# Kernel optimization log

Measured on AMD Instinct MI355X. Metric: run time of the kernel, lower is better.

## Reference

```python
import jax, jax.numpy as jnp
import numpy as np
from jax import lax

PART = 224   # PART_IMAGE_SIZE
PAD = 224    # PAD_SIZE
TOPN = 4
IOU_THRESH = 0.25
N_ANCHORS = 1614


def _conv(x, w, b, stride, pad):
    y = lax.conv_general_dilated(x, w, (stride, stride), [(pad, pad), (pad, pad)],
                                 dimension_numbers=('NCHW', 'OIHW', 'NCHW'))
    return y + b[None, :, None, None]


def _iou(box, boxes):
    # box [4], boxes [N,4] as (y0,x0,y1,x1)
    yy0 = jnp.maximum(box[0], boxes[:, 0]); xx0 = jnp.maximum(box[1], boxes[:, 1])
    yy1 = jnp.minimum(box[2], boxes[:, 2]); xx1 = jnp.minimum(box[3], boxes[:, 3])
    inter = jnp.clip(yy1 - yy0, 0.0) * jnp.clip(xx1 - xx0, 0.0)
    a = (box[2] - box[0]) * (box[3] - box[1])
    areas = (boxes[:, 2] - boxes[:, 0]) * (boxes[:, 3] - boxes[:, 1])
    return inter / (a + areas - inter)


def _nms(scores, boxes):
    # hard NMS keeping TOPN boxes; returns indices [TOPN]
    valid = jnp.ones(scores.shape, dtype=bool)
    idxs = []
    for _ in range(TOPN):
        i = jnp.argmax(jnp.where(valid, scores, -jnp.inf))
        idxs.append(i)
        valid = valid & (_iou(boxes[i], boxes) <= IOU_THRESH)
    return jnp.stack(idxs)


def _crop_resize(img, box):
    # img [3,Hp,Wp] padded image, box [4] float; bilinear, align_corners=True,
    # matching F.interpolate(x_pad[:, :, y0:y1, x0:x1], (PART, PART))
    Hp, Wp = img.shape[1], img.shape[2]
    def coords(c0, c1, L):
        t = jnp.arange(PART, dtype=img.dtype) / (PART - 1)
        c = c0 + (c1 - 1.0 - c0) * t          # absolute source coordinate
        cf = jnp.floor(c)
        lo = jnp.clip(cf.astype(jnp.int32), 0, L - 1)
        hi = jnp.clip(lo + 1, 0, L - 1)
        return lo, hi, c - cf
    yl, yh, wy = coords(box[0], box[2], Hp)
    xl, xh, wx = coords(box[1], box[3], Wp)
    g = lambda yi, xi: img[:, yi[:, None], xi[None, :]]   # [3,PART,PART]
    return ((1 - wy)[:, None] * ((1 - wx) * g(yl, xl) + wx * g(yl, xh))
            + wy[:, None] * ((1 - wx) * g(yh, xl) + wx * g(yh, xh)))


def setup_inputs() -> dict:
    key = jax.random.key(0)
    ks = jax.random.split(key, 20)
    x = jax.random.uniform(ks[0], (16, 3, 448, 448), dtype=jnp.float32)
    rpn_feature = jax.random.normal(ks[1], (16, 2048, 14, 14), dtype=jnp.float32)
    # valid boxes inside the padded 896x896 image
    y0 = jax.random.randint(ks[2], (N_ANCHORS,), 0, 560)
    x0 = jax.random.randint(ks[3], (N_ANCHORS,), 0, 560)
    h = jax.random.randint(ks[4], (N_ANCHORS,), 32, 336)
    w = jax.random.randint(ks[5], (N_ANCHORS,), 32, 336)
    anchors = jnp.stack([y0, x0, jnp.minimum(y0 + h, 896), jnp.minimum(x0 + w, 896)], axis=1).astype(jnp.int32)
    s = 0.02
    inp = {
        'x': x, 'rpn_feature': rpn_feature, 'anchors': anchors,
        'w_down1': jax.random.normal(ks[6], (128, 2048, 3, 3), jnp.float32) * s,
        'b_down1': jnp.zeros((128,), jnp.float32),
        'w_down2': jax.random.normal(ks[7], (128, 128, 3, 3), jnp.float32) * s,
        'b_down2': jnp.zeros((128,), jnp.float32),
        'w_down3': jax.random.normal(ks[8], (128, 128, 3, 3), jnp.float32) * s,
        'b_down3': jnp.zeros((128,), jnp.float32),
        'w_tidy1': jax.random.normal(ks[9], (6, 128, 1, 1), jnp.float32) * s,
        'b_tidy1': jnp.zeros((6,), jnp.float32),
        'w_tidy2': jax.random.normal(ks[10], (6, 128, 1, 1), jnp.float32) * s,
        'b_tidy2': jnp.zeros((6,), jnp.float32),
        'w_tidy3': jax.random.normal(ks[11], (9, 128, 1, 1), jnp.float32) * s,
        'b_tidy3': jnp.zeros((9,), jnp.float32),
    }
    return inp


def reference(x, rpn_feature, anchors,
              w_down1, b_down1, w_down2, b_down2, w_down3, b_down3,
              w_tidy1, b_tidy1, w_tidy2, b_tidy2, w_tidy3, b_tidy3):
    B = x.shape[0]
    # ProposalNet
    d1 = jax.nn.relu(_conv(rpn_feature, w_down1, b_down1, 1, 1))   # [B,128,14,14]
    d2 = jax.nn.relu(_conv(d1, w_down2, b_down2, 2, 1))            # [B,128,7,7]
    d3 = jax.nn.relu(_conv(d2, w_down3, b_down3, 2, 1))            # [B,128,4,4]
    t1 = _conv(d1, w_tidy1, b_tidy1, 1, 0).reshape(B, -1)
    t2 = _conv(d2, w_tidy2, b_tidy2, 1, 0).reshape(B, -1)
    t3 = _conv(d3, w_tidy3, b_tidy3, 1, 0).reshape(B, -1)
    rpn_score = jnp.concatenate([t1, t2, t3], axis=1)              # [B, 1614]
    boxes = anchors.astype(x.dtype)                                # [N,4]
    top_n_index = jax.vmap(lambda s: _nms(s, boxes))(rpn_score)    # [B,TOPN]
    top_n_prob = jnp.take_along_axis(rpn_score, top_n_index, axis=1)
    x_pad = jnp.pad(x, ((0, 0), (0, 0), (PAD, PAD), (PAD, PAD)))   # [B,3,896,896]
    sel_boxes = boxes[top_n_index]                                 # [B,TOPN,4]
    part_imgs = jax.vmap(lambda img, bxs: jax.vmap(lambda b: _crop_resize(img, b))(bxs))(x_pad, sel_boxes)
    # part_imgs: [B,TOPN,3,PART,PART]
    return rpn_score, top_n_index, top_n_prob, part_imgs
```

## Files before the change

kernel.cpp:

```cpp
#include <hip/hip_runtime.h>
#include <hip/hip_bf16.h>

#define NB 16
#define NA 1614
#define NBP (NB * 196 * 128)

typedef __bf16 bf16x8 __attribute__((ext_vector_type(8)));
typedef float f32x4 __attribute__((ext_vector_type(4)));

__device__ __forceinline__ unsigned short f2bf(float v) {
  unsigned u = __float_as_uint(v);
  unsigned r = (u + 0x7FFFu + ((u >> 16) & 1u)) >> 16;
  return (unsigned short)r;
}
__device__ __forceinline__ float bf2f(unsigned short s) {
  return __uint_as_float(((unsigned)s) << 16);
}

__global__ __launch_bounds__(256)
void prep(const float* __restrict__ w, const float* __restrict__ in,
          unsigned short* __restrict__ wTh, unsigned short* __restrict__ wTl,
          unsigned short* __restrict__ aTh, unsigned short* __restrict__ aTl) {
  __shared__ float s[32 * 201];
  const int bid = blockIdx.x;
  if (bid < 1024) {
    const int chunk = bid & 63, b = bid >> 6;
    const float* src = in + ((size_t)b * 2048 + chunk * 32) * 196;
#pragma unroll
    for (int r = 0; r < 7; r++) {
      int e = threadIdx.x + 256 * r;
      if (e < 1568) {
        int ic = e / 49, f = e - ic * 49;
        float4 v = ((const float4*)(src + (size_t)ic * 196))[f];
        float* d = s + ic * 201 + f * 4;
        d[0] = v.x; d[1] = v.y; d[2] = v.z; d[3] = v.w;
      }
    }
    __syncthreads();
    unsigned short* oh = aTh + (size_t)bid * (196 * 32);
    unsigned short* ol = aTl + (size_t)bid * (196 * 32);
#pragma unroll
    for (int r = 0; r < 4; r++) {
      int e = threadIdx.x + 256 * r;
      if (e < 784) {
        int pos = e >> 2, part = e & 3;
        unsigned short hv[8], lv[8];
#pragma unroll
        for (int j = 0; j < 8; j++) {
          float v = s[(part * 8 + j) * 201 + pos];
          unsigned short h = f2bf(v);
          hv[j] = h;
          lv[j] = f2bf(v - bf2f(h));
        }
        ((uint4*)oh)[e] = *(uint4*)hv;
        ((uint4*)ol)[e] = *(uint4*)lv;
      }
    }
  } else {
    int e = (bid - 1024) * 256 + threadIdx.x;
    if (e < 9 * 128 * 2048) {
      int tap = e / (128 * 2048);
      int rem = e - tap * (128 * 2048);
      int oc = rem >> 11, ic = rem & 2047;
      float v = w[((size_t)oc * 2048 + ic) * 9 + tap];
      unsigned short h = f2bf(v);
      wTh[e] = h;
      wTl[e] = f2bf(v - bf2f(h));
    }
  }
}

__global__ __launch_bounds__(256, 1)
void conv1_mfma(const unsigned short* __restrict__ aTh, const unsigned short* __restrict__ aTl,
                const unsigned short* __restrict__ wTh, const unsigned short* __restrict__ wTl,
                float* __restrict__ p1) {
  const int bid = blockIdx.x;
  const int kc = bid & 15;
  const int b  = bid >> 4;
  const int tid = threadIdx.x;
  const int wid = tid >> 6, lane = tid & 63;
  const int wm = wid & 1, wn = wid >> 1;
  const int q = lane >> 4, ln = lane & 15;

  __shared__ unsigned short sAh[4 * 2064];
  __shared__ unsigned short sAl[4 * 2064];
  __shared__ unsigned short sBh[4 * 1040];
  __shared__ unsigned short sBl[4 * 1040];

  for (int e = tid; e < 4128; e += 256) {
    ((unsigned int*)sAh)[e] = 0u;
    ((unsigned int*)sAl)[e] = 0u;
  }

  int abase[7];
#pragma unroll
  for (int mf = 0; mf < 7; mf++) {
    int row = wm * 112 + mf * 16 + ln;
    int y = row / 14, x = row - y * 14;
    abase[mf] = ((row < 196) ? (y * 16 + x) : 0) * 8;
  }
  const int qoff = q * 2064;

  f32x4 acc[7][4];
#pragma unroll
  for (int mf = 0; mf < 7; mf++)
#pragma unroll
    for (int nf = 0; nf < 4; nf++) acc[mf][nf] = (f32x4){0.f, 0.f, 0.f, 0.f};

  const int boc = tid >> 2, bicq = tid & 3;
  const size_t bocbase0 = (size_t)boc << 11;
  const size_t bocbase1 = (size_t)(boc + 64) << 11;

  uint4 pvh0, pvl0, pvh1, pvl1;
  {
    const size_t g = (size_t)kc * 128 + bicq * 8;
    pvh0 = *(const uint4*)(wTh + g + bocbase0);
    pvl0 = *(const uint4*)(wTl + g + bocbase0);
    pvh1 = *(const uint4*)(wTh + g + bocbase1);
    pvl1 = *(const uint4*)(wTl + g + bocbase1);
  }

  for (int it = 0; it < 36; it++) {
    const int ks = it / 9, tap = it - ks * 9;
    __syncthreads();
    *(uint4*)(sBh + bicq * 1040 + boc * 8) = pvh0;
    *(uint4*)(sBl + bicq * 1040 + boc * 8) = pvl0;
    *(uint4*)(sBh + bicq * 1040 + boc * 8 + 512) = pvh1;
    *(uint4*)(sBl + bicq * 1040 + boc * 8 + 512) = pvl1;
    if (tap == 0) {
      const uint4* gh = (const uint4*)(aTh + ((size_t)(b * 64 + kc * 4 + ks) * 196) * 32);
      const uint4* gl = (const uint4*)(aTl + ((size_t)(b * 64 + kc * 4 + ks) * 196) * 32);
#pragma unroll
      for (int r = 0; r < 4; r++) {
        int e = tid + 256 * r;
        if (e < 784) {
          int pos = e >> 2, part = e & 3;
          int py = pos / 14, px = pos - py * 14;
          int dst = part * 2064 + ((py + 1) * 16 + px + 1) * 8;
          *(uint4*)(sAh + dst) = gh[e];
          *(uint4*)(sAl + dst) = gl[e];
        }
      }
    }
    __syncthreads();
    {
      const int nit = (it < 35) ? it + 1 : 35;
      const int ks2 = nit / 9, tap2 = nit - ks2 * 9;
      const size_t g = (size_t)tap2 * (128 * 2048) + kc * 128 + ks2 * 32 + bicq * 8;
      pvh0 = *(const uint4*)(wTh + g + bocbase0);
      pvl0 = *(const uint4*)(wTl + g + bocbase0);
      pvh1 = *(const uint4*)(wTh + g + bocbase1);
      pvl1 = *(const uint4*)(wTl + g + bocbase1);
    }

    const int t8 = ((tap / 3) * 16 + (tap % 3)) * 8;
    bf16x8 bh[4], bl[4];
#pragma unroll
    for (int nf = 0; nf < 4; nf++) {
      const int bb = q * 1040 + (wn * 64 + nf * 16 + ln) * 8;
      bh[nf] = *(const bf16x8*)(sBh + bb);
      bl[nf] = *(const bf16x8*)(sBl + bb);
    }
#pragma unroll
    for (int mf = 0; mf < 7; mf++) {
      bf16x8 ah = *(const bf16x8*)(sAh + qoff + abase[mf] + t8);
      bf16x8 al = *(const bf16x8*)(sAl + qoff + abase[mf] + t8);
#pragma unroll
      for (int nf = 0; nf < 4; nf++) {
        acc[mf][nf] = __builtin_amdgcn_mfma_f32_16x16x32_bf16(ah, bh[nf], acc[mf][nf], 0, 0, 0);
        acc[mf][nf] = __builtin_amdgcn_mfma_f32_16x16x32_bf16(al, bh[nf], acc[mf][nf], 0, 0, 0);
        acc[mf][nf] = __builtin_amdgcn_mfma_f32_16x16x32_bf16(ah, bl[nf], acc[mf][nf], 0, 0, 0);
      }
    }
  }

  float* pk = p1 + ((size_t)kc * NB + b) * 196 * 128;
#pragma unroll
  for (int mf = 0; mf < 7; mf++) {
    const int row0 = wm * 112 + mf * 16 + q * 4;
#pragma unroll
    for (int nf = 0; nf < 4; nf++) {
      const int oc = wn * 64 + nf * 16 + ln;
#pragma unroll
      for (int r = 0; r < 4; r++) {
        const int row = row0 + r;
        if (row < 196) pk[(size_t)row * 128 + oc] = acc[mf][nf][r];
      }
    }
  }
}

__global__ __launch_bounds__(256)
void conv1_finish_p(const float* __restrict__ p1, const float* __restrict__ bias,
                    float* __restrict__ d1) {
  __shared__ float s[28 * 132];
  const int bid = blockIdx.x;
  const int pt = bid % 7, b = bid / 7;
  const int tid = threadIdx.x;
#pragma unroll
  for (int r = 0; r < 4; r++) {
    int u = tid + 256 * r;
    if (u < 896) {
      int pos = u >> 5, oc4 = u & 31;
      const float* base = p1 + ((size_t)(b * 196 + pt * 28 + pos)) * 128 + oc4 * 4;
      float4 sum = ((const float4*)bias)[oc4];
#pragma unroll
      for (int k = 0; k < 16; k++) {
        float4 v = *(const float4*)(base + (size_t)k * NBP);
        sum.x += v.x; sum.y += v.y; sum.z += v.z; sum.w += v.w;
      }
      sum.x = fmaxf(sum.x, 0.f); sum.y = fmaxf(sum.y, 0.f);
      sum.z = fmaxf(sum.z, 0.f); sum.w = fmaxf(sum.w, 0.f);
      *(float4*)(s + pos * 132 + oc4 * 4) = sum;
    }
  }
  __syncthreads();
#pragma unroll
  for (int r = 0; r < 4; r++) {
    int u = tid + 256 * r;
    if (u < 896) {
      int oc = u / 7, f = u - oc * 7;
      float4 v;
      v.x = s[(f * 4 + 0) * 132 + oc];
      v.y = s[(f * 4 + 1) * 132 + oc];
      v.z = s[(f * 4 + 2) * 132 + oc];
      v.w = s[(f * 4 + 3) * 132 + oc];
      *(float4*)(d1 + ((size_t)b * 128 + oc) * 196 + pt * 28 + f * 4) = v;
    }
  }
}

__global__ void conv2_part(const float* __restrict__ d1, const float* __restrict__ w,
                           float* __restrict__ p2) {
  const int bid = blockIdx.x;
  const int kc = bid & 3, oct = (bid >> 2) & 3, b = bid >> 4;
  const int ic0 = kc * 32, oc0 = oct * 32;
  const int tid = threadIdx.x;
  const int ocl = tid >> 3, rw = tid & 7;

  __shared__ float s_in[32 * 320];
  __shared__ float s_w[32 * 324];

#pragma unroll
  for (int r = 0; r < 32; r++) {
    const int e = tid + 256 * r;
    const int ch = e >> 8, idx = e & 255;
    const int tr = idx >> 4, tc = idx & 15;
    const int iy = tr - 1, ix = tc - 1;
    float v = 0.f;
    if ((unsigned)iy < 14u && (unsigned)ix < 14u)
      v = d1[((size_t)b * 128 + ic0 + ch) * 196 + iy * 14 + ix];
    s_in[ch * 320 + tr * 20 + tc] = v;
  }
#pragma unroll
  for (int r = 0; r < 36; r++) {
    const int e = tid + 256 * r;
    const int oc = e / 288, rem = e - oc * 288;
    const int ch = rem / 9, tap = rem - ch * 9;
    s_w[ch * 324 + tap * 36 + oc] =
        w[(size_t)(oc0 + oc) * 1152 + (size_t)ic0 * 9 + rem];
  }
  __syncthreads();

  if (rw < 7) {
    float acc[7] = {};
    for (int ic = 0; ic < 32; ic++) {
      const float* wrow = s_w + ic * 324 + ocl;
      const float* irow = s_in + ic * 320;
#pragma unroll
      for (int ky = 0; ky < 3; ky++) {
        const float* r = irow + (2 * rw + ky) * 20;
        const float4 f0 = *(const float4*)(r);
        const float4 f1 = *(const float4*)(r + 4);
        const float4 f2 = *(const float4*)(r + 8);
        const float4 f3 = *(const float4*)(r + 12);
        const float ev[8] = {f0.x, f0.z, f1.x, f1.z, f2.x, f2.z, f3.x, f3.z};
        const float od[7] = {f0.y, f0.w, f1.y, f1.w, f2.y, f2.w, f3.y};
        const float w0 = wrow[(ky * 3 + 0) * 36];
        const float w1 = wrow[(ky * 3 + 1) * 36];
        const float w2 = wrow[(ky * 3 + 2) * 36];
#pragma unroll
        for (int x = 0; x < 7; x++)
          acc[x] = fmaf(w0, ev[x], fmaf(w1, od[x], fmaf(w2, ev[x + 1], acc[x])));
      }
    }
    float* po = p2 + (((size_t)kc * NB + b) * 128 + oc0 + ocl) * 49 + rw * 7;
#pragma unroll
    for (int x = 0; x < 7; x++) po[x] = acc[x];
  }
}

__global__ void conv2_finish(const float* __restrict__ p2, const float* __restrict__ bias,
                             float* __restrict__ d2) {
  const int i = blockIdx.x * 256 + threadIdx.x;
  if (i >= NB * 128 * 49) return;
  const int oc = (i / 49) & 127;
  float s = bias[oc];
#pragma unroll
  for (int k = 0; k < 4; k++) s += p2[(size_t)k * (NB * 128 * 49) + i];
  d2[i] = fmaxf(s, 0.f);
}

__global__ void conv3_part(const float* __restrict__ d2, const float* __restrict__ w,
                           float* __restrict__ p3) {
  const int bid = blockIdx.x;
  const int kc = bid & 1, oct = (bid >> 1) & 7, b = bid >> 4;
  const int ic0 = kc * 64, oc0 = oct * 16;
  const int tid = threadIdx.x;
  const int oc = tid >> 4, p = tid & 15;
  const int y = p >> 2, x = p & 3;

  __shared__ float s_in[64 * 108];
  __shared__ float s_w[64 * 144];

#pragma unroll
  for (int r = 0; r < 21; r++) {
    const int e = tid + 256 * r;
    if (e < 64 * 81) {
      const int ch = e / 81, idx = e - ch * 81;
      const int tr = idx / 9, tc = idx - tr * 9;
      const int iy = tr - 1, ix = tc - 1;
      float v = 0.f;
      if ((unsigned)iy < 7u && (unsigned)ix < 7u)
        v = d2[((size_t)b * 128 + ic0 + ch) * 49 + iy * 7 + ix];
      s_in[ch * 108 + tr * 12 + tc] = v;
    }
  }
#pragma unroll
  for (int r = 0; r < 36; r++) {
    const int e = tid + 256 * r;
    const int o = e / 576, rem = e - o * 576;
    const int ch = rem / 9, tap = rem - ch * 9;
    s_w[ch * 144 + tap * 16 + o] =
        w[(size_t)(oc0 + o) * 1152 + (size_t)ic0 * 9 + rem];
  }
  __syncthreads();

  float acc = 0.f;
  for (int ic = 0; ic < 64; ic++) {
    const float* wrow = s_w + ic * 144 + oc;
    const float* irow = s_in + ic * 108 + 2 * y * 12 + 2 * x;
#pragma unroll
    for (int ky = 0; ky < 3; ky++)
#pragma unroll
      for (int kx = 0; kx < 3; kx++)
        acc = fmaf(wrow[(ky * 3 + kx) * 16], irow[ky * 12 + kx], acc);
  }
  p3[(((size_t)kc * NB + b) * 128 + oc0 + oc) * 16 + p] = acc;
}

__global__ __launch_bounds__(256, 1)
void score_nms(const float* __restrict__ d1, const float* __restrict__ d2,
               const float* __restrict__ p3, const float* __restrict__ bd3,
               const float* __restrict__ w1, const float* __restrict__ b1,
               const float* __restrict__ w2, const float* __restrict__ b2,
               const float* __restrict__ w3, const float* __restrict__ b3,
               const int* __restrict__ anchors, float* __restrict__ score,
               float* __restrict__ out_idx, float* __restrict__ out_prob,
               float* __restrict__ sel) {
  __shared__ float s_in[32 * 200];
  __shared__ float s_w[21 * 128];
  __shared__ float s_b[21];
  __shared__ float s_sc[NA];
  __shared__ float s_bx[NA * 4];
  __shared__ float r_s[256];
  __shared__ int r_i[256];
  const int b = blockIdx.x, tid = threadIdx.x;

  for (int i = tid; i < 768; i += 256) s_w[i] = w1[i];
  for (int i = tid; i < 768; i += 256) s_w[768 + i] = w2[i];
  for (int i = tid; i < 1152; i += 256) s_w[1536 + i] = w3[i];
  if (tid < 21) s_b[tid] = (tid < 6) ? b1[tid] : (tid < 12) ? b2[tid - 6] : b3[tid - 12];
  for (int i = tid; i < NA; i += 256) {
    s_bx[i * 4 + 0] = (float)anchors[i * 4 + 0];
    s_bx[i * 4 + 1] = (float)anchors[i * 4 + 1];
    s_bx[i * 4 + 2] = (float)anchors[i * 4 + 2];
    s_bx[i * 4 + 3] = (float)anchors[i * 4 + 3];
  }

  float acc[5] = {0.f, 0.f, 0.f, 0.f, 0.f};
  for (int chunk = 0; chunk < 4; chunk++) {
    __syncthreads();
    const float* src = d1 + ((size_t)b * 128 + chunk * 32) * 196;
#pragma unroll
    for (int r = 0; r < 7; r++) {
      int e = tid + 256 * r;
      if (e < 1568) {
        int ic = e / 49, f = e - ic * 49;
        *(float4*)(s_in + ic * 200 + f * 4) = ((const float4*)(src + (size_t)ic * 196))[f];
      }
    }
    __syncthreads();
#pragma unroll
    for (int k = 0; k < 5; k++) {
      int j = tid + 256 * k;
      if (j < 1176) {
        int oc = j / 196, p = j - oc * 196;
        const float* wr = s_w + oc * 128 + chunk * 32;
        float s = acc[k];
#pragma unroll
        for (int ic = 0; ic < 32; ic++) s = fmaf(wr[ic], s_in[ic * 200 + p], s);
        acc[k] = s;
      }
    }
  }
#pragma unroll
  for (int k = 0; k < 5; k++) {
    int j = tid + 256 * k;
    if (j < 1176) {
      int oc = j / 196;
      float s = acc[k] + s_b[oc];
      s_sc[j] = s;
      score[b * NA + j] = s;
    }
  }

  __syncthreads();
  {
    const float* src = d2 + (size_t)b * 6272;
#pragma unroll
    for (int r = 0; r < 7; r++) {
      int e = tid + 256 * r;
      if (e < 1568) *(float4*)(s_in + e * 4) = ((const float4*)src)[e];
    }
  }
  __syncthreads();
#pragma unroll
  for (int k = 0; k < 2; k++) {
    int jj = tid + 256 * k;
    if (jj < 294) {
      int oc = jj / 49, p = jj - oc * 49;
      const float* wr = s_w + 768 + oc * 128;
      float s = s_b[6 + oc];
#pragma unroll 8
      for (int ic = 0; ic < 128; ic++) s = fmaf(wr[ic], s_in[ic * 49 + p], s);
      s_sc[1176 + jj] = s;
      score[b * NA + 1176 + jj] = s;
    }
  }

  __syncthreads();
  {
    const float4* s0 = (const float4*)(p3 + (size_t)b * 2048);
    const float4* s1 = (const float4*)(p3 + 32768 + (size_t)b * 2048);
#pragma unroll
    for (int r = 0; r < 2; r++) {
      int e = tid + 256 * r;
      if (e < 512) {
        float4 a = s0[e], c = s1[e];
        float bb = bd3[e >> 2];
        float4 v;
        v.x = fmaxf(a.x + c.x + bb, 0.f);
        v.y = fmaxf(a.y + c.y + bb, 0.f);
        v.z = fmaxf(a.z + c.z + bb, 0.f);
        v.w = fmaxf(a.w + c.w + bb, 0.f);
        *(float4*)(s_in + e * 4) = v;
      }
    }
  }
  __syncthreads();
  if (tid < 144) {
    int oc = tid >> 4, p = tid & 15;
    const float* wr = s_w + 1536 + oc * 128;
    float s = s_b[12 + oc];
#pragma unroll 8
    for (int ic = 0; ic < 128; ic++) s = fmaf(wr[ic], s_in[ic * 16 + p], s);
    s_sc[1470 + tid] = s;
    score[b * NA + 1470 + tid] = s;
  }
  __syncthreads();

  for (int t = 0; t < 4; t++) {
    float bs = -__builtin_inff();
    int bi = NA;
    for (int i = tid; i < NA; i += 256) {
      float s = s_sc[i];
      if (s > bs || (s == bs && i < bi)) { bs = s; bi = i; }
    }
    r_s[tid] = bs; r_i[tid] = bi;
    __syncthreads();
    for (int off = 128; off > 0; off >>= 1) {
      if (tid < off) {
        float s2 = r_s[tid + off]; int i2 = r_i[tid + off];
        if (s2 > r_s[tid] || (s2 == r_s[tid] && i2 < r_i[tid])) { r_s[tid] = s2; r_i[tid] = i2; }
      }
      __syncthreads();
    }
    const int idx = r_i[0];
    const float by0 = s_bx[idx * 4 + 0], bx0 = s_bx[idx * 4 + 1];
    const float by1 = s_bx[idx * 4 + 2], bx1 = s_bx[idx * 4 + 3];
    if (tid == 0) {
      out_idx[b * 4 + t] = (float)idx;
      out_prob[b * 4 + t] = s_sc[idx];
      sel[(b * 4 + t) * 4 + 0] = by0;
      sel[(b * 4 + t) * 4 + 1] = bx0;
      sel[(b * 4 + t) * 4 + 2] = by1;
      sel[(b * 4 + t) * 4 + 3] = bx1;
    }
    __syncthreads();
    const float a = (by1 - by0) * (bx1 - bx0);
    for (int i = tid; i < NA; i += 256) {
      float cy0 = s_bx[i * 4 + 0], cx0 = s_bx[i * 4 + 1];
      float cy1 = s_bx[i * 4 + 2], cx1 = s_bx[i * 4 + 3];
      float yy0 = fmaxf(by0, cy0), xx0 = fmaxf(bx0, cx0);
      float yy1 = fminf(by1, cy1), xx1 = fminf(bx1, cx1);
      float inter = fmaxf(yy1 - yy0, 0.f) * fmaxf(xx1 - xx0, 0.f);
      float ar = (cy1 - cy0) * (cx1 - cx0);
      float iou = inter / (a + ar - inter);
      if (iou > 0.25f) s_sc[i] = -__builtin_inff();
    }
    __syncthreads();
  }
}

__global__ void crop_kernel(const float* __restrict__ x, const float* __restrict__ sel,
                            float* __restrict__ out) {
  int i4 = blockIdx.x * 256 + threadIdx.x;
  const int total4 = NB * 4 * 3 * 224 * 56;
  if (i4 >= total4) return;
  int px0 = (i4 % 56) * 4;
  int t = i4 / 56;
  int py = t % 224; t /= 224;
  int ch = t % 3;  t /= 3;
  int n  = t % 4;
  int b  = t / 4;

  const float* bx = sel + (b * 4 + n) * 4;
  const float y0 = bx[0], x0 = bx[1], y1 = bx[2], x1 = bx[3];

  float ty = (float)py / 223.0f;
  float cy = y0 + (y1 - 1.0f - y0) * ty;
  float cyf = floorf(cy);
  int ylo = (int)cyf; ylo = ylo < 0 ? 0 : (ylo > 895 ? 895 : ylo);
  int yhi = ylo + 1 > 895 ? 895 : ylo + 1;
  float wy = cy - cyf;

  const float* img = x + ((size_t)b * 3 + ch) * 448 * 448;
  auto g = [&](int yy, int xx) -> float {
    yy -= 224; xx -= 224;
    if ((unsigned)yy < 448u && (unsigned)xx < 448u)
      return img[(size_t)yy * 448 + xx];
    return 0.f;
  };

  float4 res;
  float* rp = &res.x;
#pragma unroll
  for (int k = 0; k < 4; k++) {
    float tx = (float)(px0 + k) / 223.0f;
    float cx = x0 + (x1 - 1.0f - x0) * tx;
    float cxf = floorf(cx);
    int xlo = (int)cxf; xlo = xlo < 0 ? 0 : (xlo > 895 ? 895 : xlo);
    int xhi = xlo + 1 > 895 ? 895 : xlo + 1;
    float wx = cx - cxf;
    float v00 = g(ylo, xlo), v01 = g(ylo, xhi);
    float v10 = g(yhi, xlo), v11 = g(yhi, xhi);
    rp[k] = (1.f - wy) * ((1.f - wx) * v00 + wx * v01) +
            wy * ((1.f - wx) * v10 + wx * v11);
  }
  *(float4*)(out + (size_t)i4 * 4) = res;
}

extern "C" void kernel_launch(void* const* d_in, const int* in_sizes, int n_in,
                              void* d_out, int out_size, void* d_ws, size_t ws_size,
                              hipStream_t stream) {
  const float* x    = (const float*)d_in[0];
  const float* rpn  = (const float*)d_in[1];
  const int*   anc  = (const int*)d_in[2];
  const float* w_d1 = (const float*)d_in[3];
  const float* b_d1 = (const float*)d_in[4];
  const float* w_d2 = (const float*)d_in[5];
  const float* b_d2 = (const float*)d_in[6];
  const float* w_d3 = (const float*)d_in[7];
  const float* b_d3 = (const float*)d_in[8];
  const float* w_t1 = (const float*)d_in[9];
  const float* b_t1 = (const float*)d_in[10];
  const float* w_t2 = (const float*)d_in[11];
  const float* b_t2 = (const float*)d_in[12];
  const float* w_t3 = (const float*)d_in[13];
  const float* b_t3 = (const float*)d_in[14];

  float* out = (float*)d_out;
  float* ws = (float*)d_ws;

  float* d1  = ws;
  float* d2  = d1 + 401408;
  float* d3  = d2 + 100352;
  float* sel = d3 + 32768;
  float* p2  = sel + 256;
  float* p3  = p2 + 401408;
  unsigned short* wTh = (unsigned short*)(p3 + 65536);
  unsigned short* wTl = wTh + 2359296;
  unsigned short* aTh = wTl + 2359296;
  unsigned short* aTl = aTh + 6422528;

  float* score    = out;
  float* out_idx  = out + 25824;
  float* out_prob = out + 25888;
  float* parts    = out + 25952;
  float* p1       = parts;

  prep<<<dim3(10240), dim3(256), 0, stream>>>(w_d1, rpn, wTh, wTl, aTh, aTl);
  conv1_mfma<<<dim3(256), dim3(256), 0, stream>>>(aTh, aTl, wTh, wTl, p1);
  conv1_finish_p<<<dim3(112), dim3(256), 0, stream>>>(p1, b_d1, d1);
  conv2_part<<<dim3(256), dim3(256), 0, stream>>>(d1, w_d2, p2);
  conv2_finish<<<dim3(392), dim3(256), 0, stream>>>(p2, b_d2, d2);
  conv3_part<<<dim3(256), dim3(256), 0, stream>>>(d2, w_d3, p3);
  score_nms<<<dim3(16), dim3(256), 0, stream>>>(d1, d2, p3, b_d3, w_t1, b_t1, w_t2, b_t2,
                                                w_t3, b_t3, anc, score, out_idx, out_prob, sel);
  crop_kernel<<<dim3(9408), dim3(256), 0, stream>>>(x, sel, parts);
}
```

Baseline: 285.9 us.

## Load conv1 weight fragments straight to registers and double-buffer activations in LDS

The weight prep kernel now writes the split bf16 weights in a fragment-ordered layout, so each wave loads its MFMA B operands straight from global memory into registers. This removes the LDS staging of B and the two barriers per iteration. Activation tiles are double-buffered in LDS with a padded row pitch, and the next chunk is prefetched across taps 2-6, so only one barrier per 9-tap chunk remains. The MFMA issue order is regrouped so the hi/lo products are batched. The cost is higher register pressure and repeated global loads of the weights per wave, which now depend on cache hits instead of LDS reuse.

```diff
diff --git a/kernel.cpp b/kernel.cpp
--- a/kernel.cpp
+++ b/kernel.cpp
@@ -62,13 +62,80 @@
       int tap = e / (128 * 2048);
       int rem = e - tap * (128 * 2048);
       int oc = rem >> 11, ic = rem & 2047;
+      int kcp = ic >> 7, ks = (ic >> 5) & 3, icq = (ic >> 3) & 3, j = ic & 7;
+      size_t g2 = ((size_t)(kcp * 36 + tap * 4 + ks) << 12) + oc * 32 + icq * 8 + j;
       float v = w[((size_t)oc * 2048 + ic) * 9 + tap];
       unsigned short h = f2bf(v);
-      wTh[e] = h;
-      wTl[e] = f2bf(v - bf2f(h));
-    }
-  }
-}
+      wTh[g2] = h;
+      wTl[g2] = f2bf(v - bf2f(h));
+    }
+  }
+}
+
+#define APL 2192
+#define ABUF (4 * APL)
+
+#define LOADB(H, L, T, K)                                                     \
+  {                                                                           \
+    const size_t o_ = ((size_t)(kc * 36 + (T) * 4 + (K)) << 12) + bln;        \
+    const unsigned short* ph_ = wTh + o_;                                     \
+    const unsigned short* pq_ = wTl + o_;                                     \
+    H[0] = *(const bf16x8*)(ph_);                                             \
+    H[1] = *(const bf16x8*)(ph_ + 512);                                       \
+    H[2] = *(const bf16x8*)(ph_ + 1024);                                      \
+    H[3] = *(const bf16x8*)(ph_ + 1536);                                      \
+    L[0] = *(const bf16x8*)(pq_);                                             \
+    L[1] = *(const bf16x8*)(pq_ + 512);                                       \
+    L[2] = *(const bf16x8*)(pq_ + 1024);                                      \
+    L[3] = *(const bf16x8*)(pq_ + 1536);                                      \
+  }
+
+#define STEP(IT, BUH, BUL, BNH, BNL)                                          \
+  {                                                                           \
+    const int it_ = (IT);                                                     \
+    const int ks_ = it_ / 9, tap_ = it_ - ks_ * 9;                            \
+    {             \
+      const int ni_ = (it_ < 35) ? it_ + 1 : 35;                              \
+      const int nk_ = ni_ / 9, nt_ = ni_ - nk_ * 9;                           \
+      LOADB(BNH, BNL, nt_, nk_);                                              \
+    }                                                                         \
+    if (ks_ < 3) {   \
+      const uint4* gh_ = (const uint4*)(aTh + ((size_t)(b * 64 + kc * 4 + ks_ + 1) * 196) * 32); \
+      const uint4* gl_ = (const uint4*)(aTl + ((size_t)(b * 64 + kc * 4 + ks_ + 1) * 196) * 32); \
+      if (tap_ >= 3 && tap_ <= 6) {                                           \
+        int e_ = tid + 256 * (tap_ - 3);                                      \
+        if (e_ < 784) {                                                       \
+          int pos_ = e_ >> 2, part_ = e_ & 3;                                 \
+          int py_ = pos_ / 14, px_ = pos_ - py_ * 14;                         \
+          int d_ = (((ks_ + 1) & 1) ? ABUF : 0) + part_ * APL + (py_ + 1) * 136 + (px_ + 1) * 8; \
+          *(uint4*)(sAh + d_) = sgh;                                          \
+          *(uint4*)(sAl + d_) = sgl;                                          \
+        }                                                                     \
+      }                                                                       \
+      if (tap_ >= 2 && tap_ <= 5) {                                           \
+        int e_ = tid + 256 * (tap_ - 2);                                      \
+        if (e_ < 784) { sgh = gh_[e_]; sgl = gl_[e_]; }                       \
+      }                                                                       \
+    }                                                                         \
+    const int t8_ = (tap_ / 3) * 136 + (tap_ - (tap_ / 3) * 3) * 8;           \
+    const unsigned short* pah_ = sAh + (ks_ & 1) * ABUF + qoff + t8_;         \
+    const unsigned short* pal_ = sAl + (ks_ & 1) * ABUF + qoff + t8_;         \
+    bf16x8 afh[7], afl[7];                                                    \
+    _Pragma("unroll") for (int mf = 0; mf < 7; mf++) {                        \
+      afh[mf] = *(const bf16x8*)(pah_ + abase[mf]);                           \
+      afl[mf] = *(const bf16x8*)(pal_ + abase[mf]);                           \
+    }                                                                         \
+    _Pragma("unroll") for (int mf = 0; mf < 7; mf++)                          \
+      _Pragma("unroll") for (int nf = 0; nf < 4; nf++)                        \
+        acc[mf][nf] = __builtin_amdgcn_mfma_f32_16x16x32_bf16(afh[mf], BUH[nf], acc[mf][nf], 0, 0, 0); \
+    _Pragma("unroll") for (int mf = 0; mf < 7; mf++)                          \
+      _Pragma("unroll") for (int nf = 0; nf < 4; nf++)                        \
+        acc[mf][nf] = __builtin_amdgcn_mfma_f32_16x16x32_bf16(afl[mf], BUH[nf], acc[mf][nf], 0, 0, 0); \
+    _Pragma("unroll") for (int mf = 0; mf < 7; mf++)                          \
+      _Pragma("unroll") for (int nf = 0; nf < 4; nf++)                        \
+        acc[mf][nf] = __builtin_amdgcn_mfma_f32_16x16x32_bf16(afh[mf], BUL[nf], acc[mf][nf], 0, 0, 0); \
+    if (tap_ == 8) __syncthreads();                                           \
+  }
 
 __global__ __launch_bounds__(256, 1)
 void conv1_mfma(const unsigned short* __restrict__ aTh, const unsigned short* __restrict__ aTl,
@@ -82,12 +149,10 @@
   const int wm = wid & 1, wn = wid >> 1;
   const int q = lane >> 4, ln = lane & 15;
 
-  __shared__ unsigned short sAh[4 * 2064];
-  __shared__ unsigned short sAl[4 * 2064];
-  __shared__ unsigned short sBh[4 * 1040];
-  __shared__ unsigned short sBl[4 * 1040];
-
-  for (int e = tid; e < 4128; e += 256) {
+  __shared__ unsigned short sAh[2 * ABUF];
+  __shared__ unsigned short sAl[2 * ABUF];
+
+  for (int e = tid; e < ABUF; e += 256) {
     ((unsigned int*)sAh)[e] = 0u;
     ((unsigned int*)sAl)[e] = 0u;
   }
@@ -97,9 +162,10 @@
   for (int mf = 0; mf < 7; mf++) {
     int row = wm * 112 + mf * 16 + ln;
     int y = row / 14, x = row - y * 14;
-    abase[mf] = ((row < 196) ? (y * 16 + x) : 0) * 8;
-  }
-  const int qoff = q * 2064;
+    abase[mf] = (row < 196) ? (y * 136 + x * 8) : 0;
+  }
+  const int qoff = q * APL;
+  const int bln = (wn * 64 + ln) * 32 + q * 8;
 
   f32x4 acc[7][4];
 #pragma unroll
@@ -107,71 +173,30 @@
 #pragma unroll
     for (int nf = 0; nf < 4; nf++) acc[mf][nf] = (f32x4){0.f, 0.f, 0.f, 0.f};
 
-  const int boc = tid >> 2, bicq = tid & 3;
-  const size_t bocbase0 = (size_t)boc << 11;
-  const size_t bocbase1 = (size_t)(boc + 64) << 11;
-
-  uint4 pvh0, pvl0, pvh1, pvl1;
+  uint4 sgh, sgl;
+
   {
-    const size_t g = (size_t)kc * 128 + bicq * 8;
-    pvh0 = *(const uint4*)(wTh + g + bocbase0);
-    pvl0 = *(const uint4*)(wTl + g + bocbase0);
-    pvh1 = *(const uint4*)(wTh + g + bocbase1);
-    pvl1 = *(const uint4*)(wTl + g + bocbase1);
-  }
-
-  for (int it = 0; it < 36; it++) {
-    const int ks = it / 9, tap = it - ks * 9;
-    __syncthreads();
-    *(uint4*)(sBh + bicq * 1040 + boc * 8) = pvh0;
-    *(uint4*)(sBl + bicq * 1040 + boc * 8) = pvl0;
-    *(uint4*)(sBh + bicq * 1040 + boc * 8 + 512) = pvh1;
-    *(uint4*)(sBl + bicq * 1040 + boc * 8 + 512) = pvl1;
-    if (tap == 0) {
-      const uint4* gh = (const uint4*)(aTh + ((size_t)(b * 64 + kc * 4 + ks) * 196) * 32);
-      const uint4* gl = (const uint4*)(aTl + ((size_t)(b * 64 + kc * 4 + ks) * 196) * 32);
-#pragma unroll
-      for (int r = 0; r < 4; r++) {
-        int e = tid + 256 * r;
-        if (e < 784) {
-          int pos = e >> 2, part = e & 3;
-          int py = pos / 14, px = pos - py * 14;
-          int dst = part * 2064 + ((py + 1) * 16 + px + 1) * 8;
-          *(uint4*)(sAh + dst) = gh[e];
-          *(uint4*)(sAl + dst) = gl[e];
-        }
-      }
-    }
-    __syncthreads();
-    {
-      const int nit = (it < 35) ? it + 1 : 35;
-      const int ks2 = nit / 9, tap2 = nit - ks2 * 9;
-      const size_t g = (size_t)tap2 * (128 * 2048) + kc * 128 + ks2 * 32 + bicq * 8;
-      pvh0 = *(const uint4*)(wTh + g + bocbase0);
-      pvl0 = *(const uint4*)(wTl + g + bocbase0);
-      pvh1 = *(const uint4*)(wTh + g + bocbase1);
-      pvl1 = *(const uint4*)(wTl + g + bocbase1);
-    }
-
-    const int t8 = ((tap / 3) * 16 + (tap % 3)) * 8;
-    bf16x8 bh[4], bl[4];
-#pragma unroll
-    for (int nf = 0; nf < 4; nf++) {
-      const int bb = q * 1040 + (wn * 64 + nf * 16 + ln) * 8;
-      bh[nf] = *(const bf16x8*)(sBh + bb);
-      bl[nf] = *(const bf16x8*)(sBl + bb);
-    }
-#pragma unroll
-    for (int mf = 0; mf < 7; mf++) {
-      bf16x8 ah = *(const bf16x8*)(sAh + qoff + abase[mf] + t8);
-      bf16x8 al = *(const bf16x8*)(sAl + qoff + abase[mf] + t8);
-#pragma unroll
-      for (int nf = 0; nf < 4; nf++) {
-        acc[mf][nf] = __builtin_amdgcn_mfma_f32_16x16x32_bf16(ah, bh[nf], acc[mf][nf], 0, 0, 0);
-        acc[mf][nf] = __builtin_amdgcn_mfma_f32_16x16x32_bf16(al, bh[nf], acc[mf][nf], 0, 0, 0);
-        acc[mf][nf] = __builtin_amdgcn_mfma_f32_16x16x32_bf16(ah, bl[nf], acc[mf][nf], 0, 0, 0);
-      }
-    }
+    const uint4* gh = (const uint4*)(aTh + ((size_t)(b * 64 + kc * 4) * 196) * 32);
+    const uint4* gl = (const uint4*)(aTl + ((size_t)(b * 64 + kc * 4) * 196) * 32);
+#pragma unroll
+    for (int r = 0; r < 4; r++) {
+      int e = tid + 256 * r;
+      if (e < 784) {
+        int pos = e >> 2, part = e & 3;
+        int py = pos / 14, px = pos - py * 14;
+        int d = part * APL + (py + 1) * 136 + (px + 1) * 8;
+        *(uint4*)(sAh + d) = gh[e];
+        *(uint4*)(sAl + d) = gl[e];
+      }
+    }
+  }
+  bf16x8 b0h[4], b0l[4], b1h[4], b1l[4];
+  LOADB(b0h, b0l, 0, 0);
+  __syncthreads();
+
+  for (int it = 0; it < 36; it += 2) {
+    STEP(it,     b0h, b0l, b1h, b1l);
+    STEP(it + 1, b1h, b1l, b0h, b0l);
   }
 
   float* pk = p1 + ((size_t)kc * NB + b) * 196 * 128;
```

After: 274.6 us. 1.04x faster.
